# Kernel tuning notes

Measured on AMD Instinct MI355X. Metric: run time of the kernel, lower is better.

The kernel has to match this reference:

```python
import jax, jax.numpy as jnp
import numpy as np

D_MODEL = 1024
NUM_HEADS = 16
D_K = D_MODEL // NUM_HEADS
B, S = 4, 2048


def setup_inputs() -> dict:
    key = jax.random.key(0)
    ks = jax.random.split(key, 11)
    scale = 1.0 / np.sqrt(D_MODEL)
    inp = {
        'query': jax.random.normal(ks[0], (B, S, D_MODEL), dtype=jnp.float32),
        'key':   jax.random.normal(ks[1], (B, S, D_MODEL), dtype=jnp.float32),
        'value': jax.random.normal(ks[2], (B, S, D_MODEL), dtype=jnp.float32),
        'Wq': jax.random.normal(ks[3], (D_MODEL, D_MODEL), dtype=jnp.float32) * scale,
        'bq': jnp.zeros((D_MODEL,), dtype=jnp.float32),
        'Wk': jax.random.normal(ks[4], (D_MODEL, D_MODEL), dtype=jnp.float32) * scale,
        'bk': jnp.zeros((D_MODEL,), dtype=jnp.float32),
        'Wv': jax.random.normal(ks[5], (D_MODEL, D_MODEL), dtype=jnp.float32) * scale,
        'bv': jnp.zeros((D_MODEL,), dtype=jnp.float32),
        'Wo': jax.random.normal(ks[6], (D_MODEL, D_MODEL), dtype=jnp.float32) * scale,
        'bo': jnp.zeros((D_MODEL,), dtype=jnp.float32),
    }
    return inp


def reference(query, key, value, Wq, bq, Wk, bk, Wv, bv, Wo, bo):
    b, sq, _ = query.shape
    sk = key.shape[1]
    # projections (torch Linear: x @ W.T + b; here W stored as [in, out])
    Q = query @ Wq + bq
    K = key @ Wk + bk
    V = value @ Wv + bv
    # split heads: [b, h, s, d_k]
    Q = Q.reshape(b, sq, NUM_HEADS, D_K).transpose(0, 2, 1, 3)
    K = K.reshape(b, sk, NUM_HEADS, D_K).transpose(0, 2, 1, 3)
    V = V.reshape(b, sk, NUM_HEADS, D_K).transpose(0, 2, 1, 3)
    # scaled dot-product attention (full [b,h,sq,sk] scores, as in source)
    scores = jnp.einsum('bhqd,bhkd->bhqk', Q, K) / jnp.sqrt(jnp.float32(D_K))
    attn = jax.nn.softmax(scores, axis=-1)
    out = jnp.einsum('bhqk,bhkd->bhqd', attn, V)
    out = out.transpose(0, 2, 1, 3).reshape(b, sq, D_MODEL)
    return out @ Wo + bo
```

## Files before the change

kernel.cpp:

```cpp
#include <hip/hip_runtime.h>
#include <hip/hip_bf16.h>
#include <stdint.h>

typedef __bf16 bf16x8 __attribute__((ext_vector_type(8)));
typedef __bf16 bf16x4 __attribute__((ext_vector_type(4)));
typedef float  f32x4  __attribute__((ext_vector_type(4)));
typedef unsigned short u16;

#define D_MODEL 1024
#define NUM_HEADS 16
#define DK 64
#define BATCH 4
#define SEQ 2048
#define M_TOTAL (BATCH*SEQ)
#define MD ((size_t)M_TOTAL * D_MODEL)
#define QK_SCALE 0.18033688011112042f

static __device__ __forceinline__ u16 f2bf(float f) {
    __bf16 h = (__bf16)f;
    return __builtin_bit_cast(u16, h);
}

#define ASYNC16(gptr, lptr) __builtin_amdgcn_global_load_lds( \
    (const __attribute__((address_space(1))) unsigned*)(uintptr_t)(gptr), \
    (__attribute__((address_space(3))) unsigned*)(unsigned)(uintptr_t)(lptr), 16, 0, 0)

__global__ void detect_dtype(const u16* __restrict__ q, unsigned* __restrict__ flag) {
    __shared__ int sh[256];
    int cnt = 0;
    for (int i = threadIdx.x; i < 8192; i += 256) {
        u16 v = q[2 * i];
        int e = (v >> 7) & 0xFF;
        if (e >= 100 && e <= 134) cnt++;
    }
    sh[threadIdx.x] = cnt;
    __syncthreads();
    for (int s = 128; s > 0; s >>= 1) {
        if (threadIdx.x < s) sh[threadIdx.x] += sh[threadIdx.x + s];
        __syncthreads();
    }
    if (threadIdx.x == 0) *flag = (sh[0] > 4096) ? 1u : 0u;
}

__global__ __launch_bounds__(256) void convert_bf16(
    const u16* __restrict__ q, const u16* __restrict__ k, const u16* __restrict__ v,
    u16* __restrict__ CVT, const unsigned* __restrict__ flagp)
{
    if (*flagp != 0) return;
    const int z = blockIdx.y;
    const float* src = (const float*)((z == 0) ? q : (z == 1) ? k : v);
    u16* dst = CVT + (size_t)z * MD;
    const size_t stride = (size_t)gridDim.x * 256 * 8;
    for (size_t base = ((size_t)blockIdx.x * 256 + threadIdx.x) * 8; base < MD; base += stride) {
        float4 f0 = *(const float4*)(src + base);
        float4 f1 = *(const float4*)(src + base + 4);
        bf16x8 p;
        p[0] = (__bf16)f0.x; p[1] = (__bf16)f0.y; p[2] = (__bf16)f0.z; p[3] = (__bf16)f0.w;
        p[4] = (__bf16)f1.x; p[5] = (__bf16)f1.y; p[6] = (__bf16)f1.z; p[7] = (__bf16)f1.w;
        *(bf16x8*)(dst + base) = p;
    }
}

__global__ void transpose_w(const u16* __restrict__ W0, const u16* __restrict__ W1,
                            const u16* __restrict__ W2, const u16* __restrict__ W3,
                            u16* __restrict__ WT, const unsigned* __restrict__ flagp) {
    __shared__ u16 tile[32][33];
    const u16* W = (blockIdx.z == 0) ? W0 : (blockIdx.z == 1) ? W1 : (blockIdx.z == 2) ? W2 : W3;
    u16* T = WT + (size_t)blockIdx.z * D_MODEL * D_MODEL;
    bool is_bf16 = (*flagp != 0);
    int x = threadIdx.x, y0 = threadIdx.y;
    int bx = blockIdx.x * 32, by = blockIdx.y * 32;
    if (is_bf16) {
#pragma unroll
        for (int i = 0; i < 4; i++) {
            int y = y0 + i * 8;
            tile[y][x] = W[(size_t)(by + y) * D_MODEL + bx + x];
        }
    } else {
        const float* Wf = (const float*)W;
#pragma unroll
        for (int i = 0; i < 4; i++) {
            int y = y0 + i * 8;
            tile[y][x] = f2bf(Wf[(size_t)(by + y) * D_MODEL + bx + x]);
        }
    }
    __syncthreads();
#pragma unroll
    for (int i = 0; i < 4; i++) {
        int y = y0 + i * 8;
        T[(size_t)(bx + y) * D_MODEL + by + x] = tile[x][y];
    }
}

__global__ __launch_bounds__(256) void gemm_qkv(
    const u16* __restrict__ qin, const u16* __restrict__ kin, const u16* __restrict__ vin,
    const u16* __restrict__ CVT, const u16* __restrict__ WT,
    const u16* __restrict__ bq, const u16* __restrict__ bk, const u16* __restrict__ bv,
    u16* __restrict__ Qp, u16* __restrict__ Kp, u16* __restrict__ VpT,
    const unsigned* __restrict__ flagp)
{
    __shared__ __align__(16) u16 As[128 * 64];
    __shared__ __align__(16) u16 Bs[128 * 64];

    const int id  = blockIdx.x;
    const int wg  = (id & 7) * 192 + (id >> 3);
    const int z   = wg >> 9;
    const int rr  = wg & 511;
    const int m_blk = (rr >> 3) * 128;
    const int n_blk = (rr & 7) * 128;

    const bool is_bf16 = (*flagp != 0);
    const u16* A = is_bf16 ? ((z == 0) ? qin : (z == 1) ? kin : vin)
                           : (CVT + (size_t)z * MD);
    const u16* W    = WT + (size_t)z * 1048576;
    const u16* bias = (z == 0) ? bq : (z == 1) ? bk : bv;
    u16* C          = (z == 0) ? Qp : (z == 1) ? Kp : VpT;
    const float oscale = (z == 0) ? QK_SCALE : 1.0f;

    const int tid  = threadIdx.x;
    const int lane = tid & 63, w = tid >> 6;
    const int quad = lane >> 4, l15 = lane & 15;
    const int swz  = l15 & 7;
    const int wm = w >> 1, wn = w & 1;

    const int lrow = lane >> 3;
    const int ug   = (lane & 7) ^ lrow;

    f32x4 acc[4][4] = {};

    for (int k0 = 0; k0 < D_MODEL; k0 += 64) {
#pragma unroll
        for (int i = 0; i < 4; i++) {
            const int c = w * 4 + i;
            ASYNC16(A + (size_t)(m_blk + c * 8 + lrow) * D_MODEL + k0 + ug * 8, &As[c * 512]);
            ASYNC16(W + (size_t)(n_blk + c * 8 + lrow) * D_MODEL + k0 + ug * 8, &Bs[c * 512]);
        }
        __syncthreads();

        bf16x8 a[4][2], b[4][2];
#pragma unroll
        for (int mf = 0; mf < 4; mf++)
#pragma unroll
            for (int ks = 0; ks < 2; ks++)
                a[mf][ks] = *(const bf16x8*)&As[(size_t)(wm * 64 + mf * 16 + l15) * 64
                                                + (((ks * 4 + quad) ^ swz) * 8)];
#pragma unroll
        for (int nf = 0; nf < 4; nf++)
#pragma unroll
            for (int ks = 0; ks < 2; ks++)
                b[nf][ks] = *(const bf16x8*)&Bs[(size_t)(wn * 64 + nf * 16 + l15) * 64
                                                + (((ks * 4 + quad) ^ swz) * 8)];
#pragma unroll
        for (int mf = 0; mf < 4; mf++)
#pragma unroll
            for (int nf = 0; nf < 4; nf++)
#pragma unroll
                for (int ks = 0; ks < 2; ks++)
                    acc[mf][nf] = __builtin_amdgcn_mfma_f32_16x16x32_bf16(
                        a[mf][ks], b[nf][ks], acc[mf][nf], 0, 0, 0);
        __syncthreads();
    }

#pragma unroll
    for (int nf = 0; nf < 4; nf++) {
        const int n = n_blk + wn * 64 + nf * 16 + l15;
        const float bvf = is_bf16 ? (float)((const __bf16*)bias)[n] : ((const float*)bias)[n];
#pragma unroll
        for (int mf = 0; mf < 4; mf++) {
            const int mrow = m_blk + wm * 64 + mf * 16 + quad * 4;
            if (z == 2) {
                const int bb = mrow >> 11, s = mrow & 2047;
                ushort4 pk;
                pk.x = f2bf(acc[mf][nf][0] + bvf);
                pk.y = f2bf(acc[mf][nf][1] + bvf);
                pk.z = f2bf(acc[mf][nf][2] + bvf);
                pk.w = f2bf(acc[mf][nf][3] + bvf);
                *(ushort4*)(C + (size_t)bb * D_MODEL * SEQ + (size_t)n * SEQ + s) = pk;
            } else {
#pragma unroll
                for (int r = 0; r < 4; r++)
                    C[(size_t)(mrow + r) * D_MODEL + n] = f2bf((acc[mf][nf][r] + bvf) * oscale);
            }
        }
    }
}

__global__ __launch_bounds__(256) void gemm_o(
    const u16* __restrict__ A, const u16* __restrict__ WT,
    const u16* __restrict__ bias, u16* __restrict__ C,
    const unsigned* __restrict__ flagp)
{
    __shared__ __align__(16) u16 As[128 * 64];
    __shared__ __align__(16) u16 Bs[128 * 64];

    const int id  = blockIdx.x;
    const int wg  = (id & 7) * 64 + (id >> 3);
    const int m_blk = (wg >> 3) * 128;
    const int n_blk = (wg & 7) * 128;

    const bool is_bf16 = (*flagp != 0);

    const int tid  = threadIdx.x;
    const int lane = tid & 63, w = tid >> 6;
    const int quad = lane >> 4, l15 = lane & 15;
    const int swz  = l15 & 7;
    const int wm = w >> 1, wn = w & 1;

    const int lrow = lane >> 3;
    const int ug   = (lane & 7) ^ lrow;

    f32x4 acc[4][4] = {};

    for (int k0 = 0; k0 < D_MODEL; k0 += 64) {
#pragma unroll
        for (int i = 0; i < 4; i++) {
            const int c = w * 4 + i;
            ASYNC16(A  + (size_t)(m_blk + c * 8 + lrow) * D_MODEL + k0 + ug * 8, &As[c * 512]);
            ASYNC16(WT + (size_t)(n_blk + c * 8 + lrow) * D_MODEL + k0 + ug * 8, &Bs[c * 512]);
        }
        __syncthreads();

        bf16x8 a[4][2], b[4][2];
#pragma unroll
        for (int mf = 0; mf < 4; mf++)
#pragma unroll
            for (int ks = 0; ks < 2; ks++)
                a[mf][ks] = *(const bf16x8*)&As[(size_t)(wm * 64 + mf * 16 + l15) * 64
                                                + (((ks * 4 + quad) ^ swz) * 8)];
#pragma unroll
        for (int nf = 0; nf < 4; nf++)
#pragma unroll
            for (int ks = 0; ks < 2; ks++)
                b[nf][ks] = *(const bf16x8*)&Bs[(size_t)(wn * 64 + nf * 16 + l15) * 64
                                                + (((ks * 4 + quad) ^ swz) * 8)];
#pragma unroll
        for (int mf = 0; mf < 4; mf++)
#pragma unroll
            for (int nf = 0; nf < 4; nf++)
#pragma unroll
                for (int ks = 0; ks < 2; ks++)
                    acc[mf][nf] = __builtin_amdgcn_mfma_f32_16x16x32_bf16(
                        a[mf][ks], b[nf][ks], acc[mf][nf], 0, 0, 0);
        __syncthreads();
    }

#pragma unroll
    for (int nf = 0; nf < 4; nf++) {
        const int n = n_blk + wn * 64 + nf * 16 + l15;
        const float bvf = is_bf16 ? (float)((const __bf16*)bias)[n] : ((const float*)bias)[n];
#pragma unroll
        for (int mf = 0; mf < 4; mf++) {
            const int mrow = m_blk + wm * 64 + mf * 16 + quad * 4;
            if (!is_bf16) {
                float* Cf = (float*)C;
#pragma unroll
                for (int r = 0; r < 4; r++)
                    Cf[(size_t)(mrow + r) * D_MODEL + n] = acc[mf][nf][r] + bvf;
            } else {
#pragma unroll
                for (int r = 0; r < 4; r++)
                    C[(size_t)(mrow + r) * D_MODEL + n] = f2bf(acc[mf][nf][r] + bvf);
            }
        }
    }
}

__global__ __launch_bounds__(512, 4) void attn_kernel(
    const u16* __restrict__ Qp, const u16* __restrict__ Kp,
    const u16* __restrict__ VpT, u16* __restrict__ AO)
{
    __shared__ __align__(16) u16 Ks[2][64 * 64];
    __shared__ __align__(16) u16 Vs[2][64 * 64];
    __shared__ __align__(16) u16 Ps[8][32][68];
    const int id  = blockIdx.x;
    const int xcd = id & 7, j = id >> 3;
    const int bh  = xcd * 8 + (j >> 3);
    const int qx  = j & 7;

    const int tid  = threadIdx.x;
    const int lane = tid & 63, w = tid >> 6;
    const int quad = lane >> 4, l15 = lane & 15;
    const int b = bh >> 4, h = bh & 15;
    const int q_base = qx * 256 + w * 32;

    bf16x8 bQ[2][2];
#pragma unroll
    for (int sn = 0; sn < 2; sn++)
#pragma unroll
        for (int ds = 0; ds < 2; ds++)
            bQ[sn][ds] = *(const bf16x8*)(Qp + (size_t)(b * SEQ + q_base + sn * 16 + l15) * D_MODEL
                                              + h * DK + ds * 32 + quad * 8);

    f32x4 OT[2][4] = {};
    f32x4 OTs[2]  = {};
    bf16x8 aOnes;
#pragma unroll
    for (int i = 0; i < 8; i++) aOnes[i] = (__bf16)1.0f;

    const u16* Kbase = Kp  + (size_t)(b * SEQ) * D_MODEL + h * DK;
    const u16* Vbase = VpT + (size_t)b * D_MODEL * SEQ + (size_t)(h * DK) * SEQ;

    const int lrow = lane >> 3;
    const int ug   = (lane & 7) ^ lrow;
    const int swz  = l15 & 7;

    auto issue_tile = [&](int key0, int bf) {
        ASYNC16(Kbase + (size_t)(key0 + w * 8 + lrow) * D_MODEL + ug * 8, &Ks[bf][w * 512]);
        ASYNC16(Vbase + (size_t)(w * 8 + lrow) * SEQ + key0 + ug * 8,     &Vs[bf][w * 512]);
    };

    issue_tile(0, 0);
    __syncthreads();

    for (int t = 0; t < SEQ / 64; t++) {
        const int cur = t & 1;
        if (t + 1 < SEQ / 64) issue_tile((t + 1) * 64, cur ^ 1);

#pragma unroll
        for (int kc = 0; kc < 4; kc++) {
            const int krow = (kc * 16 + l15) * 64;
            bf16x8 k0 = *(const bf16x8*)&Ks[cur][krow + ((quad ^ swz) * 8)];
            bf16x8 k1 = *(const bf16x8*)&Ks[cur][krow + (((4 + quad) ^ swz) * 8)];
#pragma unroll
            for (int sn = 0; sn < 2; sn++) {
                f32x4 s = {};
                s = __builtin_amdgcn_mfma_f32_16x16x32_bf16(k0, bQ[sn][0], s, 0, 0, 0);
                s = __builtin_amdgcn_mfma_f32_16x16x32_bf16(k1, bQ[sn][1], s, 0, 0, 0);
                bf16x4 pk;
                pk[0] = (__bf16)__builtin_amdgcn_exp2f(s[0]);
                pk[1] = (__bf16)__builtin_amdgcn_exp2f(s[1]);
                pk[2] = (__bf16)__builtin_amdgcn_exp2f(s[2]);
                pk[3] = (__bf16)__builtin_amdgcn_exp2f(s[3]);
                *(bf16x4*)&Ps[w][sn * 16 + l15][kc * 16 + quad * 4] = pk;
            }
        }

#pragma unroll
        for (int kc2 = 0; kc2 < 2; kc2++) {
            bf16x8 bP0 = *(const bf16x8*)&Ps[w][l15][kc2 * 32 + quad * 8];
            bf16x8 bP1 = *(const bf16x8*)&Ps[w][16 + l15][kc2 * 32 + quad * 8];
            OTs[0] = __builtin_amdgcn_mfma_f32_16x16x32_bf16(aOnes, bP0, OTs[0], 0, 0, 0);
            OTs[1] = __builtin_amdgcn_mfma_f32_16x16x32_bf16(aOnes, bP1, OTs[1], 0, 0, 0);
#pragma unroll
            for (int nd = 0; nd < 4; nd++) {
                bf16x8 aV = *(const bf16x8*)&Vs[cur][(nd * 16 + l15) * 64
                                                    + (((kc2 * 4 + quad) ^ swz) * 8)];
                OT[0][nd] = __builtin_amdgcn_mfma_f32_16x16x32_bf16(aV, bP0, OT[0][nd], 0, 0, 0);
                OT[1][nd] = __builtin_amdgcn_mfma_f32_16x16x32_bf16(aV, bP1, OT[1][nd], 0, 0, 0);
            }
        }
        __syncthreads();
    }

#pragma unroll
    for (int sn = 0; sn < 2; sn++) {
        float rl = 1.0f / OTs[sn][0];
        size_t rowbase = (size_t)(b * SEQ + q_base + sn * 16 + l15) * D_MODEL + h * DK;
#pragma unroll
        for (int nd = 0; nd < 4; nd++) {
            ushort4 pk;
            pk.x = f2bf(OT[sn][nd][0] * rl);
            pk.y = f2bf(OT[sn][nd][1] * rl);
            pk.z = f2bf(OT[sn][nd][2] * rl);
            pk.w = f2bf(OT[sn][nd][3] * rl);
            *(ushort4*)(AO + rowbase + nd * 16 + quad * 4) = pk;
        }
    }
}

extern "C" void kernel_launch(void* const* d_in, const int* in_sizes, int n_in,
                              void* d_out, int out_size, void* d_ws, size_t ws_size,
                              hipStream_t stream) {
    const u16* q  = (const u16*)d_in[0];
    const u16* k  = (const u16*)d_in[1];
    const u16* v  = (const u16*)d_in[2];
    const u16* Wq = (const u16*)d_in[3];
    const u16* bq = (const u16*)d_in[4];
    const u16* Wk = (const u16*)d_in[5];
    const u16* bk = (const u16*)d_in[6];
    const u16* Wv = (const u16*)d_in[7];
    const u16* bv = (const u16*)d_in[8];
    const u16* Wo = (const u16*)d_in[9];
    const u16* bo = (const u16*)d_in[10];

    u16* ws   = (u16*)d_ws;
    unsigned* flagp = (unsigned*)ws;
    u16* WT   = ws + 16;
    u16* Qp   = WT + (size_t)4 * 1024 * 1024;
    u16* Kp   = Qp + MD;
    u16* VpT  = Kp + MD;
    u16* CVT  = VpT + MD;
    u16* AO   = CVT;

    detect_dtype<<<1, 256, 0, stream>>>(q, flagp);
    convert_bf16<<<dim3(1024, 3), 256, 0, stream>>>(q, k, v, CVT, flagp);
    transpose_w<<<dim3(32, 32, 4), dim3(32, 8), 0, stream>>>(Wq, Wk, Wv, Wo, WT, flagp);
    gemm_qkv<<<1536, 256, 0, stream>>>(q, k, v, CVT, WT, bq, bk, bv, Qp, Kp, VpT, flagp);
    attn_kernel<<<512, 512, 0, stream>>>(Qp, Kp, VpT, AO);
    gemm_o<<<512, 256, 0, stream>>>(AO, WT + 3 * 1048576, bo, (u16*)d_out, flagp);
}
```

Baseline: 367.0 us.

## Fuse dtype detection, conversion and weight transpose into one prep kernel; add MFMA priority

Merges the three preprocessing launches (dtype detection, fp32-to-bf16 conversion, weight transpose) into a single kernel where every block redoes a cheap ballot-based dtype check on a sample of 256 elements, removing two launch gaps and the serial dependency on the flag. Separately wraps the MFMA sequences in the attention loop with s_setprio to raise wave priority while issuing matrix instructions. Risks are a smaller dtype-detection sample and redundant per-block sampling reads.

```diff
diff --git a/kernel.cpp b/kernel.cpp
--- a/kernel.cpp
+++ b/kernel.cpp
@@ -25,70 +25,71 @@
     (const __attribute__((address_space(1))) unsigned*)(uintptr_t)(gptr), \
     (__attribute__((address_space(3))) unsigned*)(unsigned)(uintptr_t)(lptr), 16, 0, 0)
 
-__global__ void detect_dtype(const u16* __restrict__ q, unsigned* __restrict__ flag) {
-    __shared__ int sh[256];
-    int cnt = 0;
-    for (int i = threadIdx.x; i < 8192; i += 256) {
-        u16 v = q[2 * i];
-        int e = (v >> 7) & 0xFF;
-        if (e >= 100 && e <= 134) cnt++;
-    }
-    sh[threadIdx.x] = cnt;
+__global__ __launch_bounds__(256) void prep(
+    const u16* __restrict__ q, const u16* __restrict__ k, const u16* __restrict__ v,
+    const u16* __restrict__ W0, const u16* __restrict__ W1,
+    const u16* __restrict__ W2, const u16* __restrict__ W3,
+    u16* __restrict__ WT, u16* __restrict__ CVT, unsigned* __restrict__ flagp)
+{
+    __shared__ u16 tile[32][33];
+    __shared__ int cnts[4];
+    const int tid = threadIdx.x;
+    const int lane = tid & 63, w = tid >> 6;
+
+    {
+        u16 s = q[2 * tid];
+        int e = (s >> 7) & 0xFF;
+        unsigned long long m = __ballot(e >= 100 && e <= 134);
+        if (lane == 0) cnts[w] = __popcll(m);
+    }
     __syncthreads();
-    for (int s = 128; s > 0; s >>= 1) {
-        if (threadIdx.x < s) sh[threadIdx.x] += sh[threadIdx.x + s];
-        __syncthreads();
-    }
-    if (threadIdx.x == 0) *flag = (sh[0] > 4096) ? 1u : 0u;
-}
-
-__global__ __launch_bounds__(256) void convert_bf16(
-    const u16* __restrict__ q, const u16* __restrict__ k, const u16* __restrict__ v,
-    u16* __restrict__ CVT, const unsigned* __restrict__ flagp)
-{
-    if (*flagp != 0) return;
-    const int z = blockIdx.y;
-    const float* src = (const float*)((z == 0) ? q : (z == 1) ? k : v);
-    u16* dst = CVT + (size_t)z * MD;
-    const size_t stride = (size_t)gridDim.x * 256 * 8;
-    for (size_t base = ((size_t)blockIdx.x * 256 + threadIdx.x) * 8; base < MD; base += stride) {
-        float4 f0 = *(const float4*)(src + base);
-        float4 f1 = *(const float4*)(src + base + 4);
-        bf16x8 p;
-        p[0] = (__bf16)f0.x; p[1] = (__bf16)f0.y; p[2] = (__bf16)f0.z; p[3] = (__bf16)f0.w;
-        p[4] = (__bf16)f1.x; p[5] = (__bf16)f1.y; p[6] = (__bf16)f1.z; p[7] = (__bf16)f1.w;
-        *(bf16x8*)(dst + base) = p;
-    }
-}
-
-__global__ void transpose_w(const u16* __restrict__ W0, const u16* __restrict__ W1,
-                            const u16* __restrict__ W2, const u16* __restrict__ W3,
-                            u16* __restrict__ WT, const unsigned* __restrict__ flagp) {
-    __shared__ u16 tile[32][33];
-    const u16* W = (blockIdx.z == 0) ? W0 : (blockIdx.z == 1) ? W1 : (blockIdx.z == 2) ? W2 : W3;
-    u16* T = WT + (size_t)blockIdx.z * D_MODEL * D_MODEL;
-    bool is_bf16 = (*flagp != 0);
-    int x = threadIdx.x, y0 = threadIdx.y;
-    int bx = blockIdx.x * 32, by = blockIdx.y * 32;
-    if (is_bf16) {
+    const bool is_bf16 = (cnts[0] + cnts[1] + cnts[2] + cnts[3]) > 128;
+    if (blockIdx.x == 0 && tid == 0) *flagp = is_bf16 ? 1u : 0u;
+
+    const int id = blockIdx.x;
+    if (id < 4096) {
+        const int z   = id >> 10;
+        const int rem = id & 1023;
+        const int bx = (rem & 31) * 32, by = (rem >> 5) * 32;
+        const u16* W = (z == 0) ? W0 : (z == 1) ? W1 : (z == 2) ? W2 : W3;
+        u16* T = WT + (size_t)z * D_MODEL * D_MODEL;
+        const int x = tid & 31, y0 = tid >> 5;
+        if (is_bf16) {
+#pragma unroll
+            for (int i = 0; i < 4; i++) {
+                int y = y0 + i * 8;
+                tile[y][x] = W[(size_t)(by + y) * D_MODEL + bx + x];
+            }
+        } else {
+            const float* Wf = (const float*)W;
+#pragma unroll
+            for (int i = 0; i < 4; i++) {
+                int y = y0 + i * 8;
+                tile[y][x] = f2bf(Wf[(size_t)(by + y) * D_MODEL + bx + x]);
+            }
+        }
+        __syncthreads();
 #pragma unroll
         for (int i = 0; i < 4; i++) {
             int y = y0 + i * 8;
-            tile[y][x] = W[(size_t)(by + y) * D_MODEL + bx + x];
+            T[(size_t)(bx + y) * D_MODEL + by + x] = tile[x][y];
         }
     } else {
-        const float* Wf = (const float*)W;
-#pragma unroll
-        for (int i = 0; i < 4; i++) {
-            int y = y0 + i * 8;
-            tile[y][x] = f2bf(Wf[(size_t)(by + y) * D_MODEL + bx + x]);
-        }
-    }
-    __syncthreads();
-#pragma unroll
-    for (int i = 0; i < 4; i++) {
-        int y = y0 + i * 8;
-        T[(size_t)(bx + y) * D_MODEL + by + x] = tile[x][y];
+        if (is_bf16) return;
+        const int cid = id - 4096;
+        const size_t stride = (size_t)2048 * 256 * 8;
+        const float* srcs[3] = { (const float*)q, (const float*)k, (const float*)v };
+        for (size_t idx = ((size_t)cid * 256 + tid) * 8; idx < 3 * MD; idx += stride) {
+            const int z = (int)(idx >> 23);
+            const size_t off = idx & (MD - 1);
+            const float* src = srcs[z];
+            float4 f0 = *(const float4*)(src + off);
+            float4 f1 = *(const float4*)(src + off + 4);
+            bf16x8 p;
+            p[0] = (__bf16)f0.x; p[1] = (__bf16)f0.y; p[2] = (__bf16)f0.z; p[3] = (__bf16)f0.w;
+            p[4] = (__bf16)f1.x; p[5] = (__bf16)f1.y; p[6] = (__bf16)f1.z; p[7] = (__bf16)f1.w;
+            *(bf16x8*)(CVT + (size_t)z * MD + off) = p;
+        }
     }
 }
 
@@ -324,8 +325,10 @@
 #pragma unroll
             for (int sn = 0; sn < 2; sn++) {
                 f32x4 s = {};
+                __builtin_amdgcn_s_setprio(1);
                 s = __builtin_amdgcn_mfma_f32_16x16x32_bf16(k0, bQ[sn][0], s, 0, 0, 0);
                 s = __builtin_amdgcn_mfma_f32_16x16x32_bf16(k1, bQ[sn][1], s, 0, 0, 0);
+                __builtin_amdgcn_s_setprio(0);
                 bf16x4 pk;
                 pk[0] = (__bf16)__builtin_amdgcn_exp2f(s[0]);
                 pk[1] = (__bf16)__builtin_amdgcn_exp2f(s[1]);
@@ -339,6 +342,7 @@
         for (int kc2 = 0; kc2 < 2; kc2++) {
             bf16x8 bP0 = *(const bf16x8*)&Ps[w][l15][kc2 * 32 + quad * 8];
             bf16x8 bP1 = *(const bf16x8*)&Ps[w][16 + l15][kc2 * 32 + quad * 8];
+            __builtin_amdgcn_s_setprio(1);
             OTs[0] = __builtin_amdgcn_mfma_f32_16x16x32_bf16(aOnes, bP0, OTs[0], 0, 0, 0);
             OTs[1] = __builtin_amdgcn_mfma_f32_16x16x32_bf16(aOnes, bP1, OTs[1], 0, 0, 0);
 #pragma unroll
@@ -348,6 +352,7 @@
                 OT[0][nd] = __builtin_amdgcn_mfma_f32_16x16x32_bf16(aV, bP0, OT[0][nd], 0, 0, 0);
                 OT[1][nd] = __builtin_amdgcn_mfma_f32_16x16x32_bf16(aV, bP1, OT[1][nd], 0, 0, 0);
             }
+            __builtin_amdgcn_s_setprio(0);
         }
         __syncthreads();
     }
@@ -392,9 +397,7 @@
     u16* CVT  = VpT + MD;
     u16* AO   = CVT;
 
-    detect_dtype<<<1, 256, 0, stream>>>(q, flagp);
-    convert_bf16<<<dim3(1024, 3), 256, 0, stream>>>(q, k, v, CVT, flagp);
-    transpose_w<<<dim3(32, 32, 4), dim3(32, 8), 0, stream>>>(Wq, Wk, Wv, Wo, WT, flagp);
+    prep<<<6144, 256, 0, stream>>>(q, k, v, Wq, Wk, Wv, Wo, WT, CVT, flagp);
     gemm_qkv<<<1536, 256, 0, stream>>>(q, k, v, CVT, WT, bq, bk, bv, Qp, Kp, VpT, flagp);
     attn_kernel<<<512, 512, 0, stream>>>(Qp, Kp, VpT, AO);
     gemm_o<<<512, 256, 0, stream>>>(AO, WT + 3 * 1048576, bo, (u16*)d_out, flagp);
```

Result: faster. 356.5 us (-2.9%).
